# Performance work log

Hardware: AMD Instinct MI355X
Metric: run time of the kernel (lower is better)

The kernel has to match this reference:

```python
import jax, jax.numpy as jnp
import numpy as np
from jax.scipy.special import logsumexp

NUM_CLASSES = 200
NUM_PROTOTYPES = 10
EMBED_DIM = 512
QUEUE_SIZE = 8192
MOMENTUM = 0.02
ITERATIONS = 5
EPSILON = 0.01
EPS_LOG = 1e-8


def _l2norm(x):
    return x / jnp.linalg.norm(x, axis=-1, keepdims=True)


def setup_inputs() -> dict:
    key = jax.random.key(0)
    k1, k2, k3 = jax.random.split(key, 3)
    tokens = jax.random.normal(k1, (QUEUE_SIZE, EMBED_DIM), dtype=jnp.float32)
    labels = jax.random.randint(k2, (QUEUE_SIZE,), 0, NUM_CLASSES, dtype=jnp.int64)
    # prototypes buffer is xavier-init then L2-normalized in __init__
    protos = jax.random.normal(k3, (NUM_CLASSES * NUM_PROTOTYPES, EMBED_DIM), dtype=jnp.float32)
    prototypes = _l2norm(protos)
    return {"tokens": tokens, "labels": labels, "prototypes": prototypes}


def mask_sinkhorn(C, mask, row_group_size, col_group_size, iterations, epsilon):
    # C: [P, N] cost, mask: [P, N] bool; log-domain masked Sinkhorn
    log_a = jnp.log(1.0 / row_group_size + EPS_LOG)  # [P]
    log_b = jnp.log(1.0 / col_group_size + EPS_LOG)  # [N]
    neg_inf = jnp.float32(-jnp.inf)

    def kernel(u, v):
        # (-C + u_i + v_j)/eps on mask, -inf off mask
        return jnp.where(mask, (-C + u[:, None] + v[None, :]) / epsilon, neg_inf)

    u = jnp.zeros(C.shape[0], dtype=C.dtype)
    v = jnp.zeros(C.shape[1], dtype=C.dtype)
    for _ in range(iterations):
        u_ = log_a - logsumexp(kernel(u, v), axis=1)
        u = epsilon * jnp.nan_to_num(u_, posinf=0.0) + u
        v_ = log_b - logsumexp(kernel(u, v), axis=0)
        v = epsilon * jnp.nan_to_num(v_, posinf=0.0) + v
    return jnp.exp(kernel(u, v))  # transport plan pi [P, N]


def reference(tokens, labels, prototypes):
    tok = _l2norm(tokens)  # normalize=True
    P = NUM_CLASSES * NUM_PROTOTYPES
    proto_class_id = jnp.repeat(jnp.arange(NUM_CLASSES), NUM_PROTOTYPES)  # [P]
    # group sizes (counts of same class among prototypes / among labels)
    row_group_size = jnp.full((P,), float(NUM_PROTOTYPES), dtype=jnp.float32)
    counts = jnp.bincount(labels, length=NUM_CLASSES)
    col_group_size = counts[labels].astype(jnp.float32)  # [N]
    mask = proto_class_id[:, None] == labels[None, :]  # [P, N]
    C = -(prototypes @ tok.T)  # [P, N]
    pi = mask_sinkhorn(C, mask, row_group_size, col_group_size, ITERATIONS, EPSILON)
    pi_ = pi / pi.sum(0, keepdims=True)
    new_prototypes = pi_ @ tok  # [P, D]
    out = (1.0 - MOMENTUM) * prototypes + MOMENTUM * new_prototypes
    return _l2norm(out)
```

## Files before the change

kernel.cpp:

```cpp
#include <hip/hip_runtime.h>
#include <math.h>

#define NUM_CLASSES 200
#define NUM_PROTO   10
#define EMBED_D     512
#define NTOK        8192
#define INV_EPS     100.0f
#define EPSF        0.01f
#define MOM         0.02f
#define ITERS       5
#define CAPJ        128

__device__ __forceinline__ float wave_sum(float v) {
#pragma unroll
    for (int o = 32; o; o >>= 1) v += __shfl_xor(v, o);
    return v;
}
__device__ __forceinline__ float wave_max(float v) {
#pragma unroll
    for (int o = 32; o; o >>= 1) v = fmaxf(v, __shfl_xor(v, o));
    return v;
}

__global__ __launch_bounds__(1024) void k_all(
        const float* __restrict__ tokens,
        const int*   __restrict__ labels,
        const float* __restrict__ protos,
        float*       __restrict__ out) {
    __shared__ float S_sh[NUM_PROTO][CAPJ];
    __shared__ float red[16][NUM_PROTO][128];
    __shared__ float o_sh[NUM_PROTO][EMBED_D];
    __shared__ float v_sh[CAPJ];
    __shared__ float inv_l[CAPJ];
    __shared__ float u_sh[NUM_PROTO];
    __shared__ int   idx_l[CAPJ];
    __shared__ int   weq[16];

    const int c    = blockIdx.x;
    const int tid  = threadIdx.x;
    const int lane = tid & 63;
    const int wave = tid >> 6;

    int4 la = *(const int4*)(labels + tid * 8);
    int4 lb = *(const int4*)(labels + tid * 8 + 4);
    int l[8] = {la.x, la.y, la.z, la.w, lb.x, lb.y, lb.z, lb.w};
    int meq = 0;
#pragma unroll
    for (int i = 0; i < 8; ++i) meq += (l[i] == c);
    int incl = meq;
#pragma unroll
    for (int o = 1; o < 64; o <<= 1) { int t = __shfl_up(incl, o); if (lane >= o) incl += t; }
    if (lane == 63) weq[wave] = incl;
    if (tid < CAPJ) v_sh[tid] = 0.0f;
    __syncthreads();
    int cnt = 0, wbase = 0;
#pragma unroll
    for (int w = 0; w < 16; ++w) { int q = weq[w]; cnt += q; if (w < wave) wbase += q; }
    if (cnt > CAPJ) cnt = CAPJ;
    int pos = wbase + incl - meq;
#pragma unroll
    for (int i = 0; i < 8; ++i)
        if (l[i] == c && pos < CAPJ) { idx_l[pos] = tid * 8 + i; ++pos; }
    __syncthreads();

    {
        const int wp = wave >> 1, ph = wave & 1;
        float preg[5][8];
        const float* pb = protos + (size_t)(c * NUM_PROTO + ph * 5) * EMBED_D + lane * 8;
#pragma unroll
        for (int p = 0; p < 5; ++p) {
            float4 x = *(const float4*)(pb + p * EMBED_D);
            float4 y = *(const float4*)(pb + p * EMBED_D + 4);
            preg[p][0]=x.x; preg[p][1]=x.y; preg[p][2]=x.z; preg[p][3]=x.w;
            preg[p][4]=y.x; preg[p][5]=y.y; preg[p][6]=y.z; preg[p][7]=y.w;
        }
        int j = wp;
        float4 ta, tb;
        if (j < cnt) {
            const float* tr = tokens + (size_t)idx_l[j] * EMBED_D + lane * 8;
            ta = *(const float4*)tr;
            tb = *(const float4*)(tr + 4);
        }
        while (j < cnt) {
            int j2 = j + 8;
            float4 na, nb;
            if (j2 < cnt) {
                const float* tr = tokens + (size_t)idx_l[j2] * EMBED_D + lane * 8;
                na = *(const float4*)tr;
                nb = *(const float4*)(tr + 4);
            }
            float ssq = ta.x*ta.x + ta.y*ta.y + ta.z*ta.z + ta.w*ta.w
                      + tb.x*tb.x + tb.y*tb.y + tb.z*tb.z + tb.w*tb.w;
            ssq = wave_sum(ssq);
            float inv = 1.0f / sqrtf(ssq);
            if (ph == 0 && lane == 0) inv_l[j] = inv;
#pragma unroll
            for (int p = 0; p < 5; ++p) {
                float d = preg[p][0]*ta.x + preg[p][1]*ta.y + preg[p][2]*ta.z + preg[p][3]*ta.w
                        + preg[p][4]*tb.x + preg[p][5]*tb.y + preg[p][6]*tb.z + preg[p][7]*tb.w;
                d = wave_sum(d);
                if (lane == 0) S_sh[ph * 5 + p][j] = d * inv;
            }
            ta = na; tb = nb; j = j2;
        }
    }
    __syncthreads();

    const float log_a = -2.3025850f;
    const float log_b = __logf(1.0f / (float)(cnt > 0 ? cnt : 1) + 1e-8f);
    for (int it = 0; it < ITERS; ++it) {
        if (wave < NUM_PROTO) {
            int j1 = lane + 64;
            float x0 = (lane < cnt) ? (S_sh[wave][lane] + v_sh[lane]) * INV_EPS : -1e30f;
            float x1 = (j1  < cnt) ? (S_sh[wave][j1]  + v_sh[j1])  * INV_EPS : -1e30f;
            float M  = wave_max(fmaxf(x0, x1));
            float sm = wave_sum(__expf(x0 - M) + __expf(x1 - M));
            if (lane == 0) u_sh[wave] = EPSF * (log_a - (M + __logf(sm)));
        }
        __syncthreads();
        if (it < ITERS - 1) {
            if (tid < cnt) {
                float x[NUM_PROTO], m = -1e30f;
#pragma unroll
                for (int p = 0; p < NUM_PROTO; ++p) {
                    x[p] = (S_sh[p][tid] + u_sh[p]) * INV_EPS;
                    m = fmaxf(m, x[p]);
                }
                float sm = 0.0f;
#pragma unroll
                for (int p = 0; p < NUM_PROTO; ++p) sm += __expf(x[p] - m);
                v_sh[tid] = EPSF * (log_b - (m + __logf(sm)));
            }
            __syncthreads();
        }
    }
    if (tid < cnt) {
        float x[NUM_PROTO], m = -1e30f;
#pragma unroll
        for (int p = 0; p < NUM_PROTO; ++p) {
            x[p] = (S_sh[p][tid] + u_sh[p]) * INV_EPS;
            m = fmaxf(m, x[p]);
        }
        float e[NUM_PROTO], cs = 0.0f;
#pragma unroll
        for (int p = 0; p < NUM_PROTO; ++p) { e[p] = __expf(x[p] - m); cs += e[p]; }
        float sc = inv_l[tid] / cs;
#pragma unroll
        for (int p = 0; p < NUM_PROTO; ++p) S_sh[p][tid] = e[p] * sc;
    }
    __syncthreads();

    const int g  = wave >> 2, js = wave & 3;
    const int d0 = g * 128 + lane * 2;
    float acc[NUM_PROTO][2];
#pragma unroll
    for (int p = 0; p < NUM_PROTO; ++p) { acc[p][0] = 0.0f; acc[p][1] = 0.0f; }
    for (int j = js; j < cnt; j += 4) {
        int n = idx_l[j];
        float2 t = *(const float2*)(tokens + (size_t)n * EMBED_D + d0);
#pragma unroll
        for (int p = 0; p < NUM_PROTO; ++p) {
            float w = S_sh[p][j];
            acc[p][0] += w * t.x;
            acc[p][1] += w * t.y;
        }
    }
#pragma unroll
    for (int p = 0; p < NUM_PROTO; ++p)
        *(float2*)&red[wave][p][lane * 2] = make_float2(acc[p][0], acc[p][1]);
    __syncthreads();

    for (int e4 = tid; e4 < NUM_PROTO * EMBED_D; e4 += 1024) {
        int p  = e4 >> 9;
        int d  = e4 & 511;
        int gg = d >> 7;
        int dd = d & 127;
        float s = red[gg * 4 + 0][p][dd] + red[gg * 4 + 1][p][dd]
                + red[gg * 4 + 2][p][dd] + red[gg * 4 + 3][p][dd];
        int row = c * NUM_PROTO + p;
        o_sh[p][d] = (1.0f - MOM) * protos[(size_t)row * EMBED_D + d] + MOM * s;
    }
    __syncthreads();

    if (wave < NUM_PROTO) {
        const float* orow = &o_sh[wave][0];
        float4 a = *(const float4*)(orow + lane * 8);
        float4 b = *(const float4*)(orow + lane * 8 + 4);
        float ss = a.x*a.x + a.y*a.y + a.z*a.z + a.w*a.w
                 + b.x*b.x + b.y*b.y + b.z*b.z + b.w*b.w;
        ss = wave_sum(ss);
        float inv = 1.0f / sqrtf(ss);
        int row = c * NUM_PROTO + wave;
        float* od = out + (size_t)row * EMBED_D + lane * 8;
        float4 w0 = make_float4(a.x*inv, a.y*inv, a.z*inv, a.w*inv);
        float4 w1 = make_float4(b.x*inv, b.y*inv, b.z*inv, b.w*inv);
        *(float4*)od       = w0;
        *(float4*)(od + 4) = w1;
    }
}

extern "C" void kernel_launch(void* const* d_in, const int* in_sizes, int n_in,
                              void* d_out, int out_size, void* d_ws, size_t ws_size,
                              hipStream_t stream) {
    const float* tokens = (const float*)d_in[0];
    const int*   labels = (const int*)d_in[1];
    const float* protos = (const float*)d_in[2];
    float* out = (float*)d_out;
    (void)d_ws; (void)ws_size; (void)in_sizes; (void)n_in; (void)out_size;

    k_all<<<NUM_CLASSES, 1024, 0, stream>>>(tokens, labels, protos, out);
}
```

Baseline: 33.93 us.

## Run Sinkhorn redundantly per wave in registers and batch token loads

Every wave now keeps the similarity columns for up to 128 tokens in registers and runs all Sinkhorn iterations itself with wave reductions. This removes the shared-memory u/v exchange and the per-iteration block barriers. Final weights are broadcast to the accumulation loop with shuffles instead of shared-memory reads. Token loads in the similarity and accumulation loops are batched four at a time for more memory-level parallelism. The cost is redundant exp/log work in all 16 waves and higher register pressure.

```diff
diff --git a/kernel.cpp b/kernel.cpp
--- a/kernel.cpp
+++ b/kernel.cpp
@@ -30,9 +30,7 @@
     __shared__ float S_sh[NUM_PROTO][CAPJ];
     __shared__ float red[16][NUM_PROTO][128];
     __shared__ float o_sh[NUM_PROTO][EMBED_D];
-    __shared__ float v_sh[CAPJ];
     __shared__ float inv_l[CAPJ];
-    __shared__ float u_sh[NUM_PROTO];
     __shared__ int   idx_l[CAPJ];
     __shared__ int   weq[16];
 
@@ -51,7 +49,6 @@
 #pragma unroll
     for (int o = 1; o < 64; o <<= 1) { int t = __shfl_up(incl, o); if (lane >= o) incl += t; }
     if (lane == 63) weq[wave] = incl;
-    if (tid < CAPJ) v_sh[tid] = 0.0f;
     __syncthreads();
     int cnt = 0, wbase = 0;
 #pragma unroll
@@ -74,95 +71,123 @@
             preg[p][0]=x.x; preg[p][1]=x.y; preg[p][2]=x.z; preg[p][3]=x.w;
             preg[p][4]=y.x; preg[p][5]=y.y; preg[p][6]=y.z; preg[p][7]=y.w;
         }
-        int j = wp;
-        float4 ta, tb;
-        if (j < cnt) {
-            const float* tr = tokens + (size_t)idx_l[j] * EMBED_D + lane * 8;
-            ta = *(const float4*)tr;
-            tb = *(const float4*)(tr + 4);
-        }
-        while (j < cnt) {
-            int j2 = j + 8;
-            float4 na, nb;
-            if (j2 < cnt) {
-                const float* tr = tokens + (size_t)idx_l[j2] * EMBED_D + lane * 8;
-                na = *(const float4*)tr;
-                nb = *(const float4*)(tr + 4);
-            }
-            float ssq = ta.x*ta.x + ta.y*ta.y + ta.z*ta.z + ta.w*ta.w
-                      + tb.x*tb.x + tb.y*tb.y + tb.z*tb.z + tb.w*tb.w;
-            ssq = wave_sum(ssq);
-            float inv = 1.0f / sqrtf(ssq);
-            if (ph == 0 && lane == 0) inv_l[j] = inv;
-#pragma unroll
-            for (int p = 0; p < 5; ++p) {
-                float d = preg[p][0]*ta.x + preg[p][1]*ta.y + preg[p][2]*ta.z + preg[p][3]*ta.w
-                        + preg[p][4]*tb.x + preg[p][5]*tb.y + preg[p][6]*tb.z + preg[p][7]*tb.w;
-                d = wave_sum(d);
-                if (lane == 0) S_sh[ph * 5 + p][j] = d * inv;
-            }
-            ta = na; tb = nb; j = j2;
+        for (int j0 = wp; j0 < cnt; j0 += 32) {
+            float4 A[4], B[4];
+#pragma unroll
+            for (int k = 0; k < 4; ++k) {
+                int j = j0 + 8 * k;
+                if (j < cnt) {
+                    const float* tr = tokens + (size_t)idx_l[j] * EMBED_D + lane * 8;
+                    A[k] = *(const float4*)tr;
+                    B[k] = *(const float4*)(tr + 4);
+                }
+            }
+#pragma unroll
+            for (int k = 0; k < 4; ++k) {
+                int j = j0 + 8 * k;
+                if (j < cnt) {
+                    float4 ta = A[k], tb = B[k];
+                    float ssq = ta.x*ta.x + ta.y*ta.y + ta.z*ta.z + ta.w*ta.w
+                              + tb.x*tb.x + tb.y*tb.y + tb.z*tb.z + tb.w*tb.w;
+                    ssq = wave_sum(ssq);
+                    float inv = 1.0f / sqrtf(ssq);
+                    if (ph == 0 && lane == 0) inv_l[j] = inv;
+#pragma unroll
+                    for (int p = 0; p < 5; ++p) {
+                        float d = preg[p][0]*ta.x + preg[p][1]*ta.y + preg[p][2]*ta.z + preg[p][3]*ta.w
+                                + preg[p][4]*tb.x + preg[p][5]*tb.y + preg[p][6]*tb.z + preg[p][7]*tb.w;
+                        d = wave_sum(d);
+                        if (lane == 0) S_sh[ph * 5 + p][j] = d * inv;
+                    }
+                }
+            }
         }
     }
     __syncthreads();
 
     const float log_a = -2.3025850f;
     const float log_b = __logf(1.0f / (float)(cnt > 0 ? cnt : 1) + 1e-8f);
+    const bool ok_a = lane < cnt, ok_b = lane + 64 < cnt;
+    float Sa[NUM_PROTO], Sb[NUM_PROTO], u[NUM_PROTO];
+#pragma unroll
+    for (int p = 0; p < NUM_PROTO; ++p) {
+        Sa[p] = ok_a ? S_sh[p][lane]      : -1e30f;
+        Sb[p] = ok_b ? S_sh[p][lane + 64] : -1e30f;
+    }
+    float va = 0.0f, vb = 0.0f;
     for (int it = 0; it < ITERS; ++it) {
-        if (wave < NUM_PROTO) {
-            int j1 = lane + 64;
-            float x0 = (lane < cnt) ? (S_sh[wave][lane] + v_sh[lane]) * INV_EPS : -1e30f;
-            float x1 = (j1  < cnt) ? (S_sh[wave][j1]  + v_sh[j1])  * INV_EPS : -1e30f;
-            float M  = wave_max(fmaxf(x0, x1));
-            float sm = wave_sum(__expf(x0 - M) + __expf(x1 - M));
-            if (lane == 0) u_sh[wave] = EPSF * (log_a - (M + __logf(sm)));
-        }
-        __syncthreads();
+#pragma unroll
+        for (int p = 0; p < NUM_PROTO; ++p) {
+            float xa = (Sa[p] + va) * INV_EPS;
+            float xb = (Sb[p] + vb) * INV_EPS;
+            float M  = wave_max(fmaxf(xa, xb));
+            float sm = wave_sum(__expf(xa - M) + __expf(xb - M));
+            u[p] = EPSF * (log_a - (M + __logf(sm)));
+        }
         if (it < ITERS - 1) {
-            if (tid < cnt) {
+            if (ok_a) {
                 float x[NUM_PROTO], m = -1e30f;
 #pragma unroll
-                for (int p = 0; p < NUM_PROTO; ++p) {
-                    x[p] = (S_sh[p][tid] + u_sh[p]) * INV_EPS;
-                    m = fmaxf(m, x[p]);
-                }
+                for (int p = 0; p < NUM_PROTO; ++p) { x[p] = (Sa[p] + u[p]) * INV_EPS; m = fmaxf(m, x[p]); }
                 float sm = 0.0f;
 #pragma unroll
                 for (int p = 0; p < NUM_PROTO; ++p) sm += __expf(x[p] - m);
-                v_sh[tid] = EPSF * (log_b - (m + __logf(sm)));
-            }
-            __syncthreads();
-        }
-    }
-    if (tid < cnt) {
-        float x[NUM_PROTO], m = -1e30f;
+                va = EPSF * (log_b - (m + __logf(sm)));
+            }
+            if (ok_b) {
+                float x[NUM_PROTO], m = -1e30f;
+#pragma unroll
+                for (int p = 0; p < NUM_PROTO; ++p) { x[p] = (Sb[p] + u[p]) * INV_EPS; m = fmaxf(m, x[p]); }
+                float sm = 0.0f;
+#pragma unroll
+                for (int p = 0; p < NUM_PROTO; ++p) sm += __expf(x[p] - m);
+                vb = EPSF * (log_b - (m + __logf(sm)));
+            }
+        }
+    }
+    float wa[NUM_PROTO], wb[NUM_PROTO];
+    {
+        float xa[NUM_PROTO], xb[NUM_PROTO], ma = -1e30f, mb = -1e30f;
 #pragma unroll
         for (int p = 0; p < NUM_PROTO; ++p) {
-            x[p] = (S_sh[p][tid] + u_sh[p]) * INV_EPS;
-            m = fmaxf(m, x[p]);
-        }
-        float e[NUM_PROTO], cs = 0.0f;
-#pragma unroll
-        for (int p = 0; p < NUM_PROTO; ++p) { e[p] = __expf(x[p] - m); cs += e[p]; }
-        float sc = inv_l[tid] / cs;
-#pragma unroll
-        for (int p = 0; p < NUM_PROTO; ++p) S_sh[p][tid] = e[p] * sc;
-    }
-    __syncthreads();
+            xa[p] = (Sa[p] + u[p]) * INV_EPS; ma = fmaxf(ma, xa[p]);
+            xb[p] = (Sb[p] + u[p]) * INV_EPS; mb = fmaxf(mb, xb[p]);
+        }
+        float ca = 0.0f, cb = 0.0f;
+#pragma unroll
+        for (int p = 0; p < NUM_PROTO; ++p) {
+            wa[p] = __expf(xa[p] - ma); ca += wa[p];
+            wb[p] = __expf(xb[p] - mb); cb += wb[p];
+        }
+        float sa = ok_a ? inv_l[lane]      / ca : 0.0f;
+        float sb = ok_b ? inv_l[lane + 64] / cb : 0.0f;
+#pragma unroll
+        for (int p = 0; p < NUM_PROTO; ++p) { wa[p] *= sa; wb[p] *= sb; }
+    }
 
     const int g  = wave >> 2, js = wave & 3;
     const int d0 = g * 128 + lane * 2;
     float acc[NUM_PROTO][2];
 #pragma unroll
     for (int p = 0; p < NUM_PROTO; ++p) { acc[p][0] = 0.0f; acc[p][1] = 0.0f; }
-    for (int j = js; j < cnt; j += 4) {
-        int n = idx_l[j];
-        float2 t = *(const float2*)(tokens + (size_t)n * EMBED_D + d0);
-#pragma unroll
-        for (int p = 0; p < NUM_PROTO; ++p) {
-            float w = S_sh[p][j];
-            acc[p][0] += w * t.x;
-            acc[p][1] += w * t.y;
+    for (int j0 = js; j0 < cnt; j0 += 16) {
+        float2 T[4];
+#pragma unroll
+        for (int k = 0; k < 4; ++k) {
+            int j = j0 + 4 * k;
+            if (j < cnt) T[k] = *(const float2*)(tokens + (size_t)idx_l[j] * EMBED_D + d0);
+        }
+#pragma unroll
+        for (int k = 0; k < 4; ++k) {
+            int j = j0 + 4 * k;
+            if (j < cnt) {
+#pragma unroll
+                for (int p = 0; p < NUM_PROTO; ++p) {
+                    float w = __shfl((j < 64) ? wa[p] : wb[p], j & 63);
+                    acc[p][0] += w * T[k].x;
+                    acc[p][1] += w * T[k].y;
+                }
+            }
         }
     }
 #pragma unroll
```

Result: slower. 60.28 us (+77.7%).
